# Optimization experiments

Hardware: AMD Instinct MI355X
Metric: run time of the kernel (lower is better)

## Reference

```python
import jax, jax.numpy as jnp
import numpy as np

N, F, HID, OUT, H = 4096, 128, 64, 16, 4
ALPHA = 0.2          # leaky relu slope
NEG = -9e15          # mask fill value (pyGAT convention)


def setup_inputs() -> dict:
    key = jax.random.key(0)
    ks = jax.random.split(key, 8)
    x = jax.random.normal(ks[0], (N, F), dtype=jnp.float32)
    adj = jax.random.randint(ks[1], (N, N), 0, 2, dtype=jnp.int32)
    s = lambda *sh: 0.1
    W_in = jax.random.normal(ks[2], (H, F, F), dtype=jnp.float32) * 0.1
    a_in = jax.random.normal(ks[3], (H, 2 * F), dtype=jnp.float32) * 0.1
    W_hid = jax.random.normal(ks[4], (H, F * H, HID), dtype=jnp.float32) * 0.1
    a_hid = jax.random.normal(ks[5], (H, 2 * HID), dtype=jnp.float32) * 0.1
    W_out = jax.random.normal(ks[6], (HID * H, OUT), dtype=jnp.float32) * 0.1
    a_out = jax.random.normal(ks[7], (2 * OUT,), dtype=jnp.float32) * 0.1
    return {"x": x, "adj": adj, "W_in": W_in, "a_in": a_in,
            "W_hid": W_hid, "a_hid": a_hid, "W_out": W_out, "a_out": a_out}


def _multi_head_att(x, W, a, mask):
    """Dense multi-head GAT aggregation. x:[N,Fin], W:[H,Fin,D], a:[H,2D] -> [H,N,D]."""
    D = W.shape[-1]
    h = jnp.einsum('nf,hfd->hnd', x, W)                      # [H,N,D]
    f1 = jnp.einsum('hnd,hd->hn', h, a[:, :D])               # source scores
    f2 = jnp.einsum('hnd,hd->hn', h, a[:, D:])               # target scores
    e = jax.nn.leaky_relu(f1[:, :, None] + f2[:, None, :], ALPHA)  # [H,N,N]
    e = jnp.where(mask[None, :, :], e, NEG)
    att = jax.nn.softmax(e, axis=-1)
    return jnp.einsum('hnm,hmd->hnd', att, h)                # [H,N,D]


def _concat_heads(h):
    # [H,N,D] -> [N,H*D]
    Hh, n, d = h.shape
    return jnp.transpose(h, (1, 0, 2)).reshape(n, Hh * d)


def reference(x, adj, W_in, a_in, W_hid, a_hid, W_out, a_out):
    mask = adj > 0
    # input attention block: concat=True (ELU per head), identity skip (in==out dim)
    h1 = _multi_head_att(x, W_in, a_in, mask)                # [H,N,F]
    h1 = jax.nn.elu(h1 + x[None, :, :])                      # identity residual
    h1 = _concat_heads(h1)                                   # [N,H*F]
    # hidden attention block: concat=True
    h2 = _multi_head_att(h1, W_hid, a_hid, mask)             # [H,N,HID]
    h2 = _concat_heads(jax.nn.elu(h2))                       # [N,H*HID]
    # output attention layer: single head, concat=False (no ELU inside)
    h3 = _multi_head_att(h2, W_out[None], a_out[None], mask)[0]  # [N,OUT]
    return jax.nn.log_softmax(jax.nn.elu(h3), axis=1)
```

## Files before the change

kernel.cpp:

```cpp
#include <hip/hip_runtime.h>
#include <math.h>

#define NN 4096
#define FF 128
#define HH 4
#define HIDD 64
#define OUTD 16
#define MASKW (NN / 32)
#define ALPHA 0.2f

typedef __attribute__((ext_vector_type(8))) short short8;
typedef __attribute__((ext_vector_type(4))) float f32x4;

__device__ __forceinline__ ushort f2bf(float f) {
    unsigned u = __float_as_uint(f);
    return (ushort)((u + 0x7fffu + ((u >> 16) & 1u)) >> 16);
}

__global__ void pack_mask_kernel(const int* __restrict__ adj, unsigned int* __restrict__ mb) {
    int t = blockIdx.x * 256 + threadIdx.x;
    int v = adj[t] > 0;
    unsigned long long bal = __ballot(v);
    if ((threadIdx.x & 63) == 0) {
        int w = t >> 5;
        mb[w] = (unsigned int)(bal & 0xffffffffULL);
        mb[w + 1] = (unsigned int)(bal >> 32);
    }
}

template <int FIN, int D>
__global__ __launch_bounds__(256) void proj_kernel(const float* __restrict__ A,
                                                   const float* __restrict__ W,
                                                   const float* __restrict__ av,
                                                   ushort* __restrict__ Hb,
                                                   float* __restrict__ f1,
                                                   float* __restrict__ f2) {
    constexpr int TI = 32, TF = 32;
    __shared__ float As[TI][TF + 1];
    __shared__ float Ws[TF][D];
    const int hd = blockIdx.z;
    const int i0 = blockIdx.x * TI;
    const float* Wh = W + (size_t)hd * FIN * D;
    const int t = threadIdx.x;
    const int r = t >> 3;
    const int c8 = t & 7;
    constexpr int VD = D / 8;
    float acc[VD];
#pragma unroll
    for (int k = 0; k < VD; k++) acc[k] = 0.f;
    for (int f0 = 0; f0 < FIN; f0 += TF) {
        for (int idx = t; idx < TI * TF; idx += 256) {
            int rr = idx >> 5, cc = idx & 31;
            As[rr][cc] = A[(size_t)(i0 + rr) * FIN + f0 + cc];
        }
        for (int idx = t; idx < TF * D; idx += 256) {
            int rr = idx / D, cc = idx % D;
            Ws[rr][cc] = Wh[(size_t)(f0 + rr) * D + cc];
        }
        __syncthreads();
#pragma unroll
        for (int f = 0; f < TF; f++) {
            float a = As[r][f];
#pragma unroll
            for (int k = 0; k < VD; k++) acc[k] += a * Ws[f][c8 * VD + k];
        }
        __syncthreads();
    }
    {
        const float* ah = av + hd * 2 * D;
        float s1 = 0.f, s2 = 0.f;
#pragma unroll
        for (int k = 0; k < VD; k++) {
            float hv = acc[k];
            s1 += hv * ah[c8 * VD + k];
            s2 += hv * ah[D + c8 * VD + k];
        }
#pragma unroll
        for (int o = 1; o < 8; o <<= 1) {
            s1 += __shfl_xor(s1, o);
            s2 += __shfl_xor(s2, o);
        }
        if (c8 == 0) {
            f1[hd * NN + i0 + r] = s1;
            f2[hd * NN + i0 + r] = s2;
        }
    }
    ushort* op = Hb + ((size_t)hd * NN + i0 + r) * D + c8 * VD;
#pragma unroll
    for (int k = 0; k < VD; k += 2) {
        unsigned pk = (unsigned)f2bf(acc[k]) | ((unsigned)f2bf(acc[k + 1]) << 16);
        *(unsigned*)&op[k] = pk;
    }
}

__global__ void gmax_kernel(const float* __restrict__ f2, float* __restrict__ gmax) {
    int hd = blockIdx.x;
    const float* p = f2 + (size_t)hd * NN;
    float m = -1e30f;
    for (int i = threadIdx.x; i < NN; i += 256) m = fmaxf(m, p[i]);
    __shared__ float sm[4];
#pragma unroll
    for (int off = 32; off > 0; off >>= 1) m = fmaxf(m, __shfl_down(m, off));
    if ((threadIdx.x & 63) == 0) sm[threadIdx.x >> 6] = m;
    __syncthreads();
    if (threadIdx.x == 0) gmax[hd] = fmaxf(fmaxf(sm[0], sm[1]), fmaxf(sm[2], sm[3]));
}

__global__ __launch_bounds__(256) void transpose_kernel(const ushort* __restrict__ in,
                                                        ushort* __restrict__ out, int D) {
    __shared__ ushort ts[32][33];
    const int hd = blockIdx.z;
    in += (size_t)hd * NN * D;
    out += (size_t)hd * D * NN;
    const int j0 = blockIdx.x * 32, d0 = blockIdx.y * 32;
    const int tx = threadIdx.x & 31, ty = threadIdx.x >> 5;
#pragma unroll
    for (int k = 0; k < 4; k++) {
        int row = ty + 8 * k;
        if (d0 + tx < D) ts[row][tx] = in[(size_t)(j0 + row) * D + d0 + tx];
    }
    __syncthreads();
#pragma unroll
    for (int k = 0; k < 4; k++) {
        int dr = ty + 8 * k;
        if (d0 + dr < D) out[(size_t)(d0 + dr) * NN + j0 + tx] = ts[tx][dr];
    }
}

template <int D>
__global__ __launch_bounds__(256) void agg3_kernel(const ushort* __restrict__ hT,
                                                   const float* __restrict__ f1,
                                                   const float* __restrict__ f2,
                                                   const float* __restrict__ gmax,
                                                   const unsigned int* __restrict__ mb,
                                                   float* __restrict__ pacc,
                                                   float* __restrict__ plsum) {
    constexpr int NT = D / 16;
    constexpr int NC = D / 64;
    __shared__ ushort hs[D][40];
    const int hd = blockIdx.z;
    const int js = blockIdx.y;
    const int jlen = NN / gridDim.y;
    const int jb = js * jlen, je = jb + jlen;
    const int t = threadIdx.x;
    const int w = t >> 6;
    const int lane = t & 63;
    const int ln = lane & 15;
    const int g = lane >> 4;
    const int g8 = g * 8;
    const int i0 = blockIdx.x * 64 + w * 16;
    const ushort* hTh = hT + (size_t)hd * D * NN;

    const float f1v = f1[hd * NN + i0 + ln];
    const float gm = gmax[hd];
    float mi = f1v + gm;
    mi = fmaxf(mi, ALPHA * mi);
    const float L2E = 1.442695040888963f;
    const float cexp = -mi * L2E;

    f32x4 acc[NT];
#pragma unroll
    for (int n = 0; n < NT; n++) acc[n] = (f32x4)(0.f);
    float lsum = 0.f;
    const float* f2h = f2 + hd * NN;
    const unsigned* mrow = mb + (size_t)(i0 + ln) * MASKW;

    int srow[NC], scol[NC];
#pragma unroll
    for (int c = 0; c < NC; c++) {
        int ch = t + c * 256;
        srow[c] = ch >> 2;
        scol[c] = (ch & 3) * 8;
    }
    uint4 st[NC];
#pragma unroll
    for (int c = 0; c < NC; c++)
        st[c] = *(const uint4*)&hTh[(size_t)srow[c] * NN + jb + scol[c]];
    unsigned mw = mrow[jb >> 5];
    f32x4 fA = *(const f32x4*)&f2h[jb + g8];
    f32x4 fB = *(const f32x4*)&f2h[jb + g8 + 4];

    for (int j0 = jb; j0 < je; j0 += 32) {
        __syncthreads();
#pragma unroll
        for (int c = 0; c < NC; c++) *(uint4*)&hs[srow[c]][scol[c]] = st[c];
        __syncthreads();
        const bool more = (j0 + 32) < je;
        if (more) {
#pragma unroll
            for (int c = 0; c < NC; c++)
                st[c] = *(const uint4*)&hTh[(size_t)srow[c] * NN + j0 + 32 + scol[c]];
        }
        unsigned bits = (mw >> g8) & 0xffu;
        f32x4 cA = fA, cB = fB;
        if (more) {
            mw = mrow[(j0 + 32) >> 5];
            fA = *(const f32x4*)&f2h[j0 + 32 + g8];
            fB = *(const f32x4*)&f2h[j0 + 32 + g8 + 4];
        }
        unsigned au[4];
#pragma unroll
        for (int tp = 0; tp < 4; tp++) {
            unsigned pu[2];
#pragma unroll
            for (int q = 0; q < 2; q++) {
                int tt = tp * 2 + q;
                float f2t = (tt < 4) ? cA[tt] : cB[tt - 4];
                float e = f1v + f2t;
                e = fmaxf(e, ALPHA * e);
                float p = ((bits >> tt) & 1u) ? __builtin_amdgcn_exp2f(e * L2E + cexp) : 0.f;
                pu[q] = __float_as_uint(p) & 0xffff0000u;
                lsum += __uint_as_float(pu[q]);
            }
            au[tp] = (pu[0] >> 16) | pu[1];
        }
        union { unsigned u[4]; short8 s; } aF;
#pragma unroll
        for (int q = 0; q < 4; q++) aF.u[q] = au[q];
#pragma unroll
        for (int n = 0; n < NT; n++) {
            short8 bF = *(const short8*)&hs[n * 16 + ln][g8];
            acc[n] = __builtin_amdgcn_mfma_f32_16x16x32_bf16(aF.s, bF, acc[n], 0, 0, 0);
        }
    }
    lsum += __shfl_xor(lsum, 16);
    lsum += __shfl_xor(lsum, 32);
    const size_t pbase = ((size_t)js * HH + hd) * NN;
    if (g == 0) plsum[pbase + i0 + ln] = lsum;
    float* pb = pacc + pbase * D;
#pragma unroll
    for (int n = 0; n < NT; n++) {
#pragma unroll
        for (int r = 0; r < 4; r++) {
            pb[(size_t)(i0 + g * 4 + r) * D + n * 16 + ln] = acc[n][r];
        }
    }
}

template <int D, int EPI>
__global__ __launch_bounds__(256) void combine_kernel(const float* __restrict__ pacc,
                                                      const float* __restrict__ plsum,
                                                      const float* __restrict__ xres,
                                                      float* __restrict__ out,
                                                      int ncols, int JS) {
    const int hd = blockIdx.y;
    const int e = (blockIdx.x * 256 + threadIdx.x) * 4;
    const int row = e / D;
    const int col = e % D;
    f32x4 s = (f32x4)(0.f);
    float l = 0.f;
    for (int js = 0; js < JS; js++) {
        const size_t pbase = ((size_t)js * HH + hd) * NN;
        s += *(const f32x4*)&pacc[(pbase + row) * D + col];
        l += plsum[pbase + row];
    }
    const float inv = 1.f / l;
    f32x4 xv;
    if (EPI == 1) xv = *(const f32x4*)&xres[(size_t)row * D + col];
    float* op = &out[(size_t)row * ncols + hd * D + col];
    f32x4 o;
#pragma unroll
    for (int k = 0; k < 4; k++) {
        float v = s[k] * inv;
        if (EPI == 1) v += xv[k];
        if (EPI >= 1) v = v > 0.f ? v : (__expf(v) - 1.f);
        o[k] = v;
    }
    *(f32x4*)op = o;
}

template <int D, int EPI>
__global__ __launch_bounds__(256) void agg2_kernel(const ushort* __restrict__ hT,
                                                   const float* __restrict__ f1,
                                                   const float* __restrict__ f2,
                                                   const float* __restrict__ gmax,
                                                   const unsigned int* __restrict__ mb,
                                                   const float* __restrict__ xres,
                                                   float* __restrict__ out, int ncols) {
    constexpr int NT = D / 16;
    constexpr int NC = D / 64;
    __shared__ ushort hs[D][40];
    const int hd = blockIdx.z;
    const int t = threadIdx.x;
    const int w = t >> 6;
    const int lane = t & 63;
    const int ln = lane & 15;
    const int g = lane >> 4;
    const int g8 = g * 8;
    const int i0 = blockIdx.x * 64 + w * 16;
    const ushort* hTh = hT + (size_t)hd * D * NN;
    const float f1v = f1[hd * NN + i0 + ln];
    const float gm = gmax[hd];
    float mi = f1v + gm;
    mi = fmaxf(mi, ALPHA * mi);
    const float L2E = 1.442695040888963f;
    const float cexp = -mi * L2E;
    f32x4 acc[NT];
#pragma unroll
    for (int n = 0; n < NT; n++) acc[n] = (f32x4)(0.f);
    float lsum = 0.f;
    const float* f2h = f2 + hd * NN;
    const unsigned* mrow = mb + (size_t)(i0 + ln) * MASKW;
    int srow[NC], scol[NC];
#pragma unroll
    for (int c = 0; c < NC; c++) {
        int ch = t + c * 256;
        srow[c] = ch >> 2;
        scol[c] = (ch & 3) * 8;
    }
    uint4 st[NC];
#pragma unroll
    for (int c = 0; c < NC; c++)
        st[c] = *(const uint4*)&hTh[(size_t)srow[c] * NN + scol[c]];
    unsigned mw = mrow[0];
    f32x4 fA = *(const f32x4*)&f2h[g8];
    f32x4 fB = *(const f32x4*)&f2h[g8 + 4];
    for (int j0 = 0; j0 < NN; j0 += 32) {
        __syncthreads();
#pragma unroll
        for (int c = 0; c < NC; c++) *(uint4*)&hs[srow[c]][scol[c]] = st[c];
        __syncthreads();
        const bool more = (j0 + 32) < NN;
        if (more) {
#pragma unroll
            for (int c = 0; c < NC; c++)
                st[c] = *(const uint4*)&hTh[(size_t)srow[c] * NN + j0 + 32 + scol[c]];
        }
        unsigned bits = (mw >> g8) & 0xffu;
        f32x4 cA = fA, cB = fB;
        if (more) {
            mw = mrow[(j0 + 32) >> 5];
            fA = *(const f32x4*)&f2h[j0 + 32 + g8];
            fB = *(const f32x4*)&f2h[j0 + 32 + g8 + 4];
        }
        unsigned au[4];
#pragma unroll
        for (int tp = 0; tp < 4; tp++) {
            unsigned pu[2];
#pragma unroll
            for (int q = 0; q < 2; q++) {
                int tt = tp * 2 + q;
                float f2t = (tt < 4) ? cA[tt] : cB[tt - 4];
                float e = f1v + f2t;
                e = fmaxf(e, ALPHA * e);
                float p = ((bits >> tt) & 1u) ? __builtin_amdgcn_exp2f(e * L2E + cexp) : 0.f;
                pu[q] = __float_as_uint(p) & 0xffff0000u;
                lsum += __uint_as_float(pu[q]);
            }
            au[tp] = (pu[0] >> 16) | pu[1];
        }
        union { unsigned u[4]; short8 s; } aF;
#pragma unroll
        for (int q = 0; q < 4; q++) aF.u[q] = au[q];
#pragma unroll
        for (int n = 0; n < NT; n++) {
            short8 bF = *(const short8*)&hs[n * 16 + ln][g8];
            acc[n] = __builtin_amdgcn_mfma_f32_16x16x32_bf16(aF.s, bF, acc[n], 0, 0, 0);
        }
    }
    lsum += __shfl_xor(lsum, 16);
    lsum += __shfl_xor(lsum, 32);
    const float linv = 1.f / lsum;
#pragma unroll
    for (int n = 0; n < NT; n++) {
#pragma unroll
        for (int r = 0; r < 4; r++) {
            float invr = __shfl(linv, (g << 2) + r);
            float v = acc[n][r] * invr;
            int row = i0 + g * 4 + r;
            int col = n * 16 + ln;
            if (EPI == 1) v += xres[(size_t)row * D + col];
            if (EPI >= 1) v = v > 0.f ? v : (__expf(v) - 1.f);
            out[(size_t)row * ncols + hd * D + col] = v;
        }
    }
}

template <int D, int EPI, int NW>
__global__ __launch_bounds__(NW * 64) void agg_mfma_kernel(const ushort* __restrict__ hT,
                                                           const float* __restrict__ f1,
                                                           const float* __restrict__ f2,
                                                           const float* __restrict__ gmax,
                                                           const unsigned int* __restrict__ mb,
                                                           const float* __restrict__ xres,
                                                           float* __restrict__ out, int ncols) {
    constexpr int NT = D / 16;
    static_assert(NW == 1 || NT == 1, "j-split only for single-tile D");
    const int hd = blockIdx.z;
    const int i0 = blockIdx.x * 16;
    const int w = threadIdx.x >> 6;
    const int lane = threadIdx.x & 63;
    const int ln = lane & 15;
    const int g = lane >> 4;
    const int g8 = g * 8;
    const ushort* hTh = hT + (size_t)hd * D * NN;
    const float f1v = f1[hd * NN + i0 + ln];
    const float gm = gmax[hd];
    float mi = f1v + gm;
    mi = fmaxf(mi, ALPHA * mi);
    f32x4 acc[NT];
#pragma unroll
    for (int n = 0; n < NT; n++) acc[n] = (f32x4)(0.f);
    float lsum = 0.f;
    const float* f2h = f2 + hd * NN;
    const unsigned* mrow = mb + (size_t)(i0 + ln) * MASKW;
    const int jbeg = w * (NN / NW), jend = jbeg + NN / NW;

    for (int j0 = jbeg; j0 < jend; j0 += 32) {
        unsigned bits = (mrow[j0 >> 5] >> g8) & 0xffu;
        f32x4 fA = *(const f32x4*)&f2h[j0 + g8];
        f32x4 fB = *(const f32x4*)&f2h[j0 + g8 + 4];
        short8 aF;
#pragma unroll
        for (int t = 0; t < 8; t++) {
            float f2t = (t < 4) ? fA[t] : fB[t - 4];
            float e = f1v + f2t;
            e = fmaxf(e, ALPHA * e);
            float p = ((bits >> t) & 1u) ? __expf(e - mi) : 0.f;
            ushort pb = f2bf(p);
            aF[t] = (short)pb;
            lsum += __uint_as_float((unsigned)pb << 16);
        }
#pragma unroll
        for (int n = 0; n < NT; n++) {
            short8 bF = *(const short8*)&hTh[(size_t)(n * 16 + ln) * NN + j0 + g8];
            acc[n] = __builtin_amdgcn_mfma_f32_16x16x32_bf16(aF, bF, acc[n], 0, 0, 0);
        }
    }
    lsum += __shfl_xor(lsum, 16);
    lsum += __shfl_xor(lsum, 32);

    float accF[NT][4];
    float ltot;
    __shared__ float accL[NW][16][17];
    __shared__ float lsL[NW][16];
    if constexpr (NW == 1) {
#pragma unroll
        for (int n = 0; n < NT; n++)
#pragma unroll
            for (int r = 0; r < 4; r++) accF[n][r] = acc[n][r];
        ltot = lsum;
    } else {
#pragma unroll
        for (int r = 0; r < 4; r++) accL[w][g * 4 + r][ln] = acc[0][r];
        if (lane < 16) lsL[w][lane] = lsum;
        __syncthreads();
        if (w != 0) return;
#pragma unroll
        for (int r = 0; r < 4; r++) {
            float s = 0.f;
            for (int ww = 0; ww < NW; ww++) s += accL[ww][g * 4 + r][ln];
            accF[0][r] = s;
        }
        float s = 0.f;
        for (int ww = 0; ww < NW; ww++) s += lsL[ww][ln];
        ltot = s;
    }
    const float linv = 1.f / ltot;
#pragma unroll
    for (int n = 0; n < NT; n++) {
#pragma unroll
        for (int r = 0; r < 4; r++) {
            float invr = __shfl(linv, (g << 2) + r);
            float v = accF[n][r] * invr;
            int row = i0 + g * 4 + r;
            int col = n * 16 + ln;
            if (EPI == 1) v += xres[(size_t)row * D + col];
            if (EPI >= 1) v = v > 0.f ? v : (__expf(v) - 1.f);
            out[(size_t)row * ncols + hd * D + col] = v;
        }
    }
}

__global__ void final_kernel(const float* __restrict__ h3, float* __restrict__ out) {
    int i = blockIdx.x * 256 + threadIdx.x;
    if (i >= NN) return;
    float v[OUTD];
    float mx = -1e30f;
#pragma unroll
    for (int k = 0; k < OUTD; k++) {
        float e = h3[(size_t)i * OUTD + k];
        e = e > 0.f ? e : (__expf(e) - 1.f);
        v[k] = e;
        mx = fmaxf(mx, e);
    }
    float s = 0.f;
#pragma unroll
    for (int k = 0; k < OUTD; k++) s += __expf(v[k] - mx);
    float ls = logf(s);
#pragma unroll
    for (int k = 0; k < OUTD; k++) out[(size_t)i * OUTD + k] = v[k] - mx - ls;
}

extern "C" void kernel_launch(void* const* d_in, const int* in_sizes, int n_in,
                              void* d_out, int out_size, void* d_ws, size_t ws_size,
                              hipStream_t stream) {
    const float* x = (const float*)d_in[0];
    const int* adj = (const int*)d_in[1];
    const float* W_in = (const float*)d_in[2];
    const float* a_in = (const float*)d_in[3];
    const float* W_hid = (const float*)d_in[4];
    const float* a_hid = (const float*)d_in[5];
    const float* W_out = (const float*)d_in[6];
    const float* a_out = (const float*)d_in[7];
    float* out = (float*)d_out;

    char* w = (char*)d_ws;
    unsigned int* mb = (unsigned int*)w;  w += (size_t)NN * MASKW * 4;
    ushort* hb16 = (ushort*)w;            w += (size_t)HH * NN * FF * 2;
    ushort* hT = (ushort*)w;              w += (size_t)HH * NN * FF * 2;
    float* cat1 = (float*)w;              w += (size_t)NN * (HH * FF) * 4;
    float* f1 = (float*)w;                w += (size_t)HH * NN * 4;
    float* f2 = (float*)w;                w += (size_t)HH * NN * 4;
    float* gm = (float*)w;                w += 256;
    float* h3 = (float*)w;                w += (size_t)NN * OUTD * 4;
    float* cat2 = cat1;
    size_t base_used = (size_t)(w - (char*)d_ws);

    int JS = 0;
    float* pacc = (float*)w;
    float* plsum = nullptr;
    {
        size_t per_js = (size_t)HH * NN * FF * 4;
        size_t ls_per_js = (size_t)HH * NN * 4;
        for (int cand = 4; cand >= 1; cand >>= 1) {
            size_t need = base_used + (size_t)cand * per_js + (size_t)(2 * cand) * ls_per_js + 1024;
            if (ws_size >= need) { JS = cand; break; }
        }
        if (JS) plsum = (float*)((char*)pacc + (size_t)JS * per_js);
    }
    const int JS2 = 2 * JS;

    hipLaunchKernelGGL(pack_mask_kernel, dim3(NN * NN / 256), dim3(256), 0, stream, adj, mb);

    hipLaunchKernelGGL((proj_kernel<FF, FF>), dim3(NN / 32, 1, HH), dim3(256), 0, stream,
                       x, W_in, a_in, hb16, f1, f2);
    hipLaunchKernelGGL(gmax_kernel, dim3(HH), dim3(256), 0, stream, f2, gm);
    hipLaunchKernelGGL(transpose_kernel, dim3(NN / 32, FF / 32, HH), dim3(256), 0, stream, hb16, hT, FF);
    if (JS) {
        hipLaunchKernelGGL((agg3_kernel<FF>), dim3(NN / 64, JS, HH), dim3(256), 0, stream,
                           hT, f1, f2, gm, mb, pacc, plsum);
        hipLaunchKernelGGL((combine_kernel<FF, 1>), dim3(NN * FF / 1024, HH), dim3(256), 0, stream,
                           pacc, plsum, x, cat1, HH * FF, JS);
    } else {
        hipLaunchKernelGGL((agg2_kernel<FF, 1>), dim3(NN / 64, 1, HH), dim3(256), 0, stream,
                           hT, f1, f2, gm, mb, x, cat1, HH * FF);
    }

    hipLaunchKernelGGL((proj_kernel<HH * FF, HIDD>), dim3(NN / 32, 1, HH), dim3(256), 0, stream,
                       cat1, W_hid, a_hid, hb16, f1, f2);
    hipLaunchKernelGGL(gmax_kernel, dim3(HH), dim3(256), 0, stream, f2, gm);
    hipLaunchKernelGGL(transpose_kernel, dim3(NN / 32, HIDD / 32, HH), dim3(256), 0, stream, hb16, hT, HIDD);
    if (JS) {
        hipLaunchKernelGGL((agg3_kernel<HIDD>), dim3(NN / 64, JS2, HH), dim3(256), 0, stream,
                           hT, f1, f2, gm, mb, pacc, plsum);
        hipLaunchKernelGGL((combine_kernel<HIDD, 2>), dim3(NN * HIDD / 1024, HH), dim3(256), 0, stream,
                           pacc, plsum, (const float*)nullptr, cat2, HH * HIDD, JS2);
    } else {
        hipLaunchKernelGGL((agg2_kernel<HIDD, 2>), dim3(NN / 64, 1, HH), dim3(256), 0, stream,
                           hT, f1, f2, gm, mb, (const float*)nullptr, cat2, HH * HIDD);
    }

    hipLaunchKernelGGL((proj_kernel<HH * HIDD, OUTD>), dim3(NN / 32, 1, 1), dim3(256), 0, stream,
                       cat2, W_out, a_out, hb16, f1, f2);
    hipLaunchKernelGGL(gmax_kernel, dim3(1), dim3(256), 0, stream, f2, gm);
    hipLaunchKernelGGL(transpose_kernel, dim3(NN / 32, 1, 1), dim3(256), 0, stream, hb16, hT, OUTD);
    hipLaunchKernelGGL((agg_mfma_kernel<OUTD, 0, 4>), dim3(NN / 16, 1, 1), dim3(256), 0, stream,
                       hT, f1, f2, gm, mb, (const float*)nullptr, h3, OUTD);

    hipLaunchKernelGGL(final_kernel, dim3(NN / 256), dim3(256), 0, stream, h3, out);
}
```

Baseline: 388.4 us.

## Replace fp32 projection GEMMs with bf16 MFMA kernels writing transposed output

Replaces the scalar fp32 tiled projection kernel with a bf16 MFMA kernel that writes the transposed feature matrix directly, which removes the separate transpose pass. Attention scores f1/f2 are now computed separately as dot products of the layer input with precomputed W·a vectors. Intermediate concatenated activations are stored as bf16, and weights are pre-transposed and converted once per call. This cuts FP32 ALU work and memory traffic at the cost of extra small prep launches and reduced precision in the intermediates and scores.

Result: faster. 339.3 us (-12.6%).

```diff
diff --git a/kernel.cpp b/kernel.cpp
--- a/kernel.cpp
+++ b/kernel.cpp
@@ -15,6 +15,9 @@
 __device__ __forceinline__ ushort f2bf(float f) {
     unsigned u = __float_as_uint(f);
     return (ushort)((u + 0x7fffu + ((u >> 16) & 1u)) >> 16);
+}
+__device__ __forceinline__ float bf2f(ushort u) {
+    return __uint_as_float((unsigned)u << 16);
 }
 
 __global__ void pack_mask_kernel(const int* __restrict__ adj, unsigned int* __restrict__ mb) {
@@ -28,69 +31,89 @@
     }
 }
 
-template <int FIN, int D>
-__global__ __launch_bounds__(256) void proj_kernel(const float* __restrict__ A,
-                                                   const float* __restrict__ W,
-                                                   const float* __restrict__ av,
-                                                   ushort* __restrict__ Hb,
-                                                   float* __restrict__ f1,
-                                                   float* __restrict__ f2) {
-    constexpr int TI = 32, TF = 32;
-    __shared__ float As[TI][TF + 1];
-    __shared__ float Ws[TF][D];
-    const int hd = blockIdx.z;
-    const int i0 = blockIdx.x * TI;
-    const float* Wh = W + (size_t)hd * FIN * D;
-    const int t = threadIdx.x;
-    const int r = t >> 3;
-    const int c8 = t & 7;
-    constexpr int VD = D / 8;
-    float acc[VD];
-#pragma unroll
-    for (int k = 0; k < VD; k++) acc[k] = 0.f;
-    for (int f0 = 0; f0 < FIN; f0 += TF) {
-        for (int idx = t; idx < TI * TF; idx += 256) {
-            int rr = idx >> 5, cc = idx & 31;
-            As[rr][cc] = A[(size_t)(i0 + rr) * FIN + f0 + cc];
-        }
-        for (int idx = t; idx < TF * D; idx += 256) {
-            int rr = idx / D, cc = idx % D;
-            Ws[rr][cc] = Wh[(size_t)(f0 + rr) * D + cc];
-        }
-        __syncthreads();
-#pragma unroll
-        for (int f = 0; f < TF; f++) {
-            float a = As[r][f];
-#pragma unroll
-            for (int k = 0; k < VD; k++) acc[k] += a * Ws[f][c8 * VD + k];
-        }
-        __syncthreads();
-    }
-    {
-        const float* ah = av + hd * 2 * D;
-        float s1 = 0.f, s2 = 0.f;
-#pragma unroll
-        for (int k = 0; k < VD; k++) {
-            float hv = acc[k];
-            s1 += hv * ah[c8 * VD + k];
-            s2 += hv * ah[D + c8 * VD + k];
-        }
-#pragma unroll
-        for (int o = 1; o < 8; o <<= 1) {
-            s1 += __shfl_xor(s1, o);
-            s2 += __shfl_xor(s2, o);
-        }
-        if (c8 == 0) {
-            f1[hd * NN + i0 + r] = s1;
-            f2[hd * NN + i0 + r] = s2;
-        }
-    }
-    ushort* op = Hb + ((size_t)hd * NN + i0 + r) * D + c8 * VD;
-#pragma unroll
-    for (int k = 0; k < VD; k += 2) {
-        unsigned pk = (unsigned)f2bf(acc[k]) | ((unsigned)f2bf(acc[k + 1]) << 16);
-        *(unsigned*)&op[k] = pk;
-    }
+__global__ void cvt_kernel(const float* __restrict__ x, ushort* __restrict__ xb) {
+    int e = (blockIdx.x * 256 + threadIdx.x) * 4;
+    f32x4 v = *(const f32x4*)&x[e];
+    unsigned lo = (unsigned)f2bf(v[0]) | ((unsigned)f2bf(v[1]) << 16);
+    unsigned hi = (unsigned)f2bf(v[2]) | ((unsigned)f2bf(v[3]) << 16);
+    uint2 p; p.x = lo; p.y = hi;
+    *(uint2*)&xb[e] = p;
+}
+
+__global__ void wtprep_kernel(const float* __restrict__ W_in, const float* __restrict__ W_hid,
+                              const float* __restrict__ W_out,
+                              ushort* __restrict__ wt1, ushort* __restrict__ wt2,
+                              ushort* __restrict__ wt3) {
+    int idx = blockIdx.x * 256 + threadIdx.x;
+    if (idx < 65536) {
+        int k = idx & 127, n = (idx >> 7) & 127, hd = idx >> 14;
+        wt1[idx] = f2bf(W_in[((size_t)hd * 128 + k) * 128 + n]);
+    } else if (idx < 65536 + 131072) {
+        int j = idx - 65536;
+        int k = j & 511, n = (j >> 9) & 63, hd = j >> 15;
+        wt2[j] = f2bf(W_hid[((size_t)hd * 512 + k) * 64 + n]);
+    } else if (idx < 65536 + 131072 + 4096) {
+        int j = idx - 196608;
+        int k = j & 255, n = j >> 8;
+        wt3[j] = f2bf(W_out[(size_t)k * 16 + n]);
+    }
+}
+
+__global__ void vprep_kernel(const float* __restrict__ W_in, const float* __restrict__ a_in,
+                             const float* __restrict__ W_hid, const float* __restrict__ a_hid,
+                             const float* __restrict__ W_out, const float* __restrict__ a_out,
+                             float* __restrict__ vbuf) {
+    int idx = blockIdx.x * 256 + threadIdx.x;
+    const float* Wr; const float* ar; int D; float* dst;
+    if (idx < 1024) {
+        int f = idx & 127, hd = (idx >> 7) & 3, s = idx >> 9;
+        Wr = W_in + ((size_t)hd * 128 + f) * 128;
+        ar = a_in + hd * 256 + s * 128;
+        D = 128; dst = &vbuf[idx];
+    } else if (idx < 1024 + 4096) {
+        int j = idx - 1024;
+        int f = j & 511, hd = (j >> 9) & 3, s = j >> 11;
+        Wr = W_hid + ((size_t)hd * 512 + f) * 64;
+        ar = a_hid + hd * 128 + s * 64;
+        D = 64; dst = &vbuf[1024 + j];
+    } else if (idx < 1024 + 4096 + 512) {
+        int j = idx - 5120;
+        int f = j & 255, s = j >> 8;
+        Wr = W_out + (size_t)f * 16;
+        ar = a_out + s * 16;
+        D = 16; dst = &vbuf[5120 + j];
+    } else return;
+    float s = 0.f;
+    for (int d = 0; d < D; d++) s += Wr[d] * ar[d];
+    *dst = s;
+}
+
+template <typename T, int K, int H>
+__global__ __launch_bounds__(256) void score_kernel(const T* __restrict__ A,
+                                                    const float* __restrict__ v,
+                                                    float* __restrict__ f1,
+                                                    float* __restrict__ f2) {
+    int wv = blockIdx.x * 4 + (threadIdx.x >> 6);
+    int lane = threadIdx.x & 63;
+    int hd = wv >> 12;
+    int i = wv & (NN - 1);
+    const T* ar = A + (size_t)i * K;
+    const float* v1r = v + (size_t)hd * K;
+    const float* v2r = v + (size_t)(H + hd) * K;
+    float s1 = 0.f, s2 = 0.f;
+    for (int f = lane; f < K; f += 64) {
+        float av;
+        if constexpr (sizeof(T) == 2) av = bf2f(((const ushort*)ar)[f]);
+        else av = ((const float*)ar)[f];
+        s1 += av * v1r[f];
+        s2 += av * v2r[f];
+    }
+#pragma unroll
+    for (int o = 32; o > 0; o >>= 1) {
+        s1 += __shfl_down(s1, o);
+        s2 += __shfl_down(s2, o);
+    }
+    if (lane == 0) { f1[wv] = s1; f2[wv] = s2; }
 }
 
 __global__ void gmax_kernel(const float* __restrict__ f2, float* __restrict__ gmax) {
@@ -106,24 +129,44 @@
     if (threadIdx.x == 0) gmax[hd] = fmaxf(fmaxf(sm[0], sm[1]), fmaxf(sm[2], sm[3]));
 }
 
-__global__ __launch_bounds__(256) void transpose_kernel(const ushort* __restrict__ in,
-                                                        ushort* __restrict__ out, int D) {
-    __shared__ ushort ts[32][33];
-    const int hd = blockIdx.z;
-    in += (size_t)hd * NN * D;
-    out += (size_t)hd * D * NN;
-    const int j0 = blockIdx.x * 32, d0 = blockIdx.y * 32;
-    const int tx = threadIdx.x & 31, ty = threadIdx.x >> 5;
-#pragma unroll
-    for (int k = 0; k < 4; k++) {
-        int row = ty + 8 * k;
-        if (d0 + tx < D) ts[row][tx] = in[(size_t)(j0 + row) * D + d0 + tx];
-    }
-    __syncthreads();
-#pragma unroll
-    for (int k = 0; k < 4; k++) {
-        int dr = ty + 8 * k;
-        if (d0 + dr < D) out[(size_t)(d0 + dr) * NN + j0 + tx] = ts[tx][dr];
+template <int K, int N, int CFG>
+__global__ __launch_bounds__(256) void proj_mfma_kernel(const ushort* __restrict__ A,
+                                                        const ushort* __restrict__ WT,
+                                                        ushort* __restrict__ hT) {
+    constexpr int NT = (CFG == 0) ? (N / 64) : (N / 16);
+    __shared__ ushort ts[4][NT * 16][20];
+    const int hd = blockIdx.y;
+    const int t = threadIdx.x;
+    const int w = t >> 6, lane = t & 63, ln = lane & 15, g = lane >> 4, g8 = g * 8;
+    const int i0 = (CFG == 0) ? blockIdx.x * 16 : blockIdx.x * 64 + w * 16;
+    const int n0 = (CFG == 0) ? w * (N / 4) : 0;
+    const ushort* WTh = WT + (size_t)hd * N * K;
+    ushort* hTh = hT + (size_t)hd * N * NN;
+    f32x4 acc[NT];
+#pragma unroll
+    for (int n = 0; n < NT; n++) acc[n] = (f32x4)(0.f);
+    const ushort* arow = A + (size_t)(i0 + ln) * K + g8;
+#pragma unroll
+    for (int k0 = 0; k0 < K; k0 += 32) {
+        short8 aF = *(const short8*)&arow[k0];
+#pragma unroll
+        for (int n = 0; n < NT; n++) {
+            short8 bF = *(const short8*)&WTh[(size_t)(n0 + n * 16 + ln) * K + k0 + g8];
+            acc[n] = __builtin_amdgcn_mfma_f32_16x16x32_bf16(aF, bF, acc[n], 0, 0, 0);
+        }
+    }
+#pragma unroll
+    for (int n = 0; n < NT; n++) {
+        unsigned lo = (unsigned)f2bf(acc[n][0]) | ((unsigned)f2bf(acc[n][1]) << 16);
+        unsigned hi = (unsigned)f2bf(acc[n][2]) | ((unsigned)f2bf(acc[n][3]) << 16);
+        uint2 p; p.x = lo; p.y = hi;
+        *(uint2*)&ts[w][n * 16 + ln][g * 4] = p;
+    }
+#pragma unroll
+    for (int n = 0; n < NT; n++) {
+        int d = lane >> 2, ip = lane & 3;
+        uint2 rv = *(uint2*)&ts[w][n * 16 + d][ip * 4];
+        *(uint2*)&hTh[(size_t)(n0 + n * 16 + d) * NN + i0 + ip * 4] = rv;
     }
 }
 
@@ -241,7 +284,7 @@
 __global__ __launch_bounds__(256) void combine_kernel(const float* __restrict__ pacc,
                                                       const float* __restrict__ plsum,
                                                       const float* __restrict__ xres,
-                                                      float* __restrict__ out,
+                                                      ushort* __restrict__ out,
                                                       int ncols, int JS) {
     const int hd = blockIdx.y;
     const int e = (blockIdx.x * 256 + threadIdx.x) * 4;
@@ -257,8 +300,7 @@
     const float inv = 1.f / l;
     f32x4 xv;
     if (EPI == 1) xv = *(const f32x4*)&xres[(size_t)row * D + col];
-    float* op = &out[(size_t)row * ncols + hd * D + col];
-    f32x4 o;
+    float o[4];
 #pragma unroll
     for (int k = 0; k < 4; k++) {
         float v = s[k] * inv;
@@ -266,7 +308,10 @@
         if (EPI >= 1) v = v > 0.f ? v : (__expf(v) - 1.f);
         o[k] = v;
     }
-    *(f32x4*)op = o;
+    unsigned lo = (unsigned)f2bf(o[0]) | ((unsigned)f2bf(o[1]) << 16);
+    unsigned hi = (unsigned)f2bf(o[2]) | ((unsigned)f2bf(o[3]) << 16);
+    uint2 p; p.x = lo; p.y = hi;
+    *(uint2*)&out[(size_t)row * ncols + hd * D + col] = p;
 }
 
 template <int D, int EPI>
@@ -276,7 +321,7 @@
                                                    const float* __restrict__ gmax,
                                                    const unsigned int* __restrict__ mb,
                                                    const float* __restrict__ xres,
-                                                   float* __restrict__ out, int ncols) {
+                                                   ushort* __restrict__ out, int ncols) {
     constexpr int NT = D / 16;
     constexpr int NC = D / 64;
     __shared__ ushort hs[D][40];
@@ -371,7 +416,7 @@
             int col = n * 16 + ln;
             if (EPI == 1) v += xres[(size_t)row * D + col];
             if (EPI >= 1) v = v > 0.f ? v : (__expf(v) - 1.f);
-            out[(size_t)row * ncols + hd * D + col] = v;
+            out[(size_t)row * ncols + hd * D + col] = f2bf(v);
         }
     }
 }
@@ -507,14 +552,18 @@
 
     char* w = (char*)d_ws;
     unsigned int* mb = (unsigned int*)w;  w += (size_t)NN * MASKW * 4;
-    ushort* hb16 = (ushort*)w;            w += (size_t)HH * NN * FF * 2;
     ushort* hT = (ushort*)w;              w += (size_t)HH * NN * FF * 2;
-    float* cat1 = (float*)w;              w += (size_t)NN * (HH * FF) * 4;
+    ushort* xb16 = (ushort*)w;            w += (size_t)NN * FF * 2;
+    ushort* cat1b = (ushort*)w;           w += (size_t)NN * (HH * FF) * 2;
+    ushort* cat2b = (ushort*)w;           w += (size_t)NN * (HH * HIDD) * 2;
+    ushort* wt1 = (ushort*)w;             w += 65536 * 2;
+    ushort* wt2 = (ushort*)w;             w += 131072 * 2;
+    ushort* wt3 = (ushort*)w;             w += 4096 * 2;
+    float* vbuf = (float*)w;              w += 5632 * 4;
     float* f1 = (float*)w;                w += (size_t)HH * NN * 4;
     float* f2 = (float*)w;                w += (size_t)HH * NN * 4;
     float* gm = (float*)w;                w += 256;
     float* h3 = (float*)w;                w += (size_t)NN * OUTD * 4;
-    float* cat2 = cat1;
     size_t base_used = (size_t)(w - (char*)d_ws);
 
     int JS = 0;
@@ -532,39 +581,47 @@
     const int JS2 = 2 * JS;
 
     hipLaunchKernelGGL(pack_mask_kernel, dim3(NN * NN / 256), dim3(256), 0, stream, adj, mb);
-
-    hipLaunchKernelGGL((proj_kernel<FF, FF>), dim3(NN / 32, 1, HH), dim3(256), 0, stream,
-                       x, W_in, a_in, hb16, f1, f2);
+    hipLaunchKernelGGL(cvt_kernel, dim3(NN * FF / 1024), dim3(256), 0, stream, x, xb16);
+    hipLaunchKernelGGL(wtprep_kernel, dim3(784), dim3(256), 0, stream,
+                       W_in, W_hid, W_out, wt1, wt2, wt3);
+    hipLaunchKernelGGL(vprep_kernel, dim3(22), dim3(256), 0, stream,
+                       W_in, a_in, W_hid, a_hid, W_out, a_out, vbuf);
+
+    hipLaunchKernelGGL((proj_mfma_kernel<FF, FF, 0>), dim3(NN / 16, HH), dim3(256), 0, stream,
+                       xb16, wt1, hT);
+    hipLaunchKernelGGL((score_kernel<float, FF, HH>), dim3(HH * NN / 4), dim3(256), 0, stream,
+                       x, vbuf, f1, f2);
     hipLaunchKernelGGL(gmax_kernel, dim3(HH), dim3(256), 0, stream, f2, gm);
-    hipLaunchKernelGGL(transpose_kernel, dim3(NN / 32, FF / 32, HH), dim3(256), 0, stream, hb16, hT, FF);
     if (JS) {
         hipLaunchKernelGGL((agg3_kernel<FF>), dim3(NN / 64, JS, HH), dim3(256), 0, stream,
                            hT, f1, f2, gm, mb, pacc, plsum);
         hipLaunchKernelGGL((combine_kernel<FF, 1>), dim3(NN * FF / 1024, HH), dim3(256), 0, stream,
-                           pacc, plsum, x, cat1, HH * FF, JS);
+                           pacc, plsum, x, cat1b, HH * FF, JS);
     } else {
         hipLaunchKernelGGL((agg2_kernel<FF, 1>), dim3(NN / 64, 1, HH), dim3(256), 0, stream,
-                           hT, f1, f2, gm, mb, x, cat1, HH * FF);
-    }
-
-    hipLaunchKernelGGL((proj_kernel<HH * FF, HIDD>), dim3(NN / 32, 1, HH), dim3(256), 0, stream,
-                       cat1, W_hid, a_hid, hb16, f1, f2);
+                           hT, f1, f2, gm, mb, x, cat1b, HH * FF);
+    }
+
+    hipLaunchKernelGGL((proj_mfma_kernel<HH * FF, HIDD, 0>), dim3(NN / 16, HH), dim3(256), 0, stream,
+                       cat1b, wt2, hT);
+    hipLaunchKernelGGL((score_kernel<ushort, HH * FF, HH>), dim3(HH * NN / 4), dim3(256), 0, stream,
+                       cat1b, vbuf + 1024, f1, f2);
     hipLaunchKernelGGL(gmax_kernel, dim3(HH), dim3(256), 0, stream, f2, gm);
-    hipLaunchKernelGGL(transpose_kernel, dim3(NN / 32, HIDD / 32, HH), dim3(256), 0, stream, hb16, hT, HIDD);
     if (JS) {
         hipLaunchKernelGGL((agg3_kernel<HIDD>), dim3(NN / 64, JS2, HH), dim3(256), 0, stream,
                            hT, f1, f2, gm, mb, pacc, plsum);
         hipLaunchKernelGGL((combine_kernel<HIDD, 2>), dim3(NN * HIDD / 1024, HH), dim3(256), 0, stream,
-                           pacc, plsum, (const float*)nullptr, cat2, HH * HIDD, JS2);
+                           pacc, plsum, (const float*)nullptr, cat2b, HH * HIDD, JS2);
     } else {
         hipLaunchKernelGGL((agg2_kernel<HIDD, 2>), dim3(NN / 64, 1, HH), dim3(256), 0, stream,
-                           hT, f1, f2, gm, mb, (const float*)nullptr, cat2, HH * HIDD);
-    }
-
-    hipLaunchKernelGGL((proj_kernel<HH * HIDD, OUTD>), dim3(NN / 32, 1, 1), dim3(256), 0, stream,
-                       cat2, W_out, a_out, hb16, f1, f2);
+                           hT, f1, f2, gm, mb, (const float*)nullptr, cat2b, HH * HIDD);
+    }
+
+    hipLaunchKernelGGL((proj_mfma_kernel<HH * HIDD, OUTD, 1>), dim3(NN / 64, 1), dim3(256), 0, stream,
+                       cat2b, wt3, hT);
+    hipLaunchKernelGGL((score_kernel<ushort, HH * HIDD, 1>), dim3(NN / 4), dim3(256), 0, stream,
+                       cat2b, vbuf + 5120, f1, f2);
     hipLaunchKernelGGL(gmax_kernel, dim3(1), dim3(256), 0, stream, f2, gm);
-    hipLaunchKernelGGL(transpose_kernel, dim3(NN / 32, 1, 1), dim3(256), 0, stream, hb16, hT, OUTD);
     hipLaunchKernelGGL((agg_mfma_kernel<OUTD, 0, 4>), dim3(NN / 16, 1, 1), dim3(256), 0, stream,
                        hT, f1, f2, gm, mb, (const float*)nullptr, h3, OUTD);
 
```
